# Optimization experiments

Hardware: AMD Instinct MI355X
Metric: run time of the kernel (lower is better)

Reference implementation:

```python
import jax, jax.numpy as jnp
import numpy as np

STRIDE = 4.0      # fpn_strides[0]
POOL = 7          # roi_align_size
SR = 2            # roi_align_sampling_ratio
NUM_CLASSES = 10
B, N = 2, 512
C, H, W = 256, 256, 256
OUT = 1024


def _bilinear(feat_hwc, y, x):
    # feat_hwc: [H, W, C]; y, x: [N, 7, 7, SR, SR] sample coords (feature units)
    Hf, Wf, _ = feat_hwc.shape
    valid = (y > -1.0) & (y < Hf) & (x > -1.0) & (x < Wf)
    y = jnp.clip(y, 0.0, Hf - 1.0)
    x = jnp.clip(x, 0.0, Wf - 1.0)
    y0 = jnp.floor(y)
    x0 = jnp.floor(x)
    y0i = y0.astype(jnp.int32)
    x0i = x0.astype(jnp.int32)
    y1i = jnp.minimum(y0i + 1, Hf - 1)
    x1i = jnp.minimum(x0i + 1, Wf - 1)
    ly = (y - y0)[..., None]
    lx = (x - x0)[..., None]
    hy = 1.0 - ly
    hx = 1.0 - lx
    v = (hy * hx * feat_hwc[y0i, x0i] + hy * lx * feat_hwc[y0i, x1i]
         + ly * hx * feat_hwc[y1i, x0i] + ly * lx * feat_hwc[y1i, x1i])
    return v * valid[..., None]


def _roi_align_rotated(feat_hwc, boxes):
    # boxes: [N, 5] = (cx, cy, w, h, theta) in feature coords -> [N, 7, 7, C]
    cx, cy, w, h, th = (boxes[:, k] for k in range(5))
    bins = jnp.arange(POOL, dtype=feat_hwc.dtype)
    sub = (jnp.arange(SR, dtype=feat_hwc.dtype) + 0.5) / SR
    # local (box-frame) coords of sample points along each axis: [N, 7, SR]
    ys = -h[:, None, None] / 2 + (h / POOL)[:, None, None] * (bins[None, :, None] + sub[None, None, :])
    xs = -w[:, None, None] / 2 + (w / POOL)[:, None, None] * (bins[None, :, None] + sub[None, None, :])
    yy = ys[:, :, None, :, None]  # [N,7,1,SR,1]
    xx = xs[:, None, :, None, :]  # [N,1,7,1,SR]
    cos = jnp.cos(th)[:, None, None, None, None]
    sin = jnp.sin(th)[:, None, None, None, None]
    gx = cx[:, None, None, None, None] + xx * cos - yy * sin
    gy = cy[:, None, None, None, None] + xx * sin + yy * cos
    v = _bilinear(feat_hwc, gy, gx)  # [N,7,7,SR,SR,C]
    return v.mean(axis=(3, 4))       # average-pool the SRxSR samples per bin


def norm_angle(a):
    return (a + jnp.pi / 2) % jnp.pi - jnp.pi / 2


def setup_inputs():
    key = jax.random.key(0)
    ks = jax.random.split(key, 14)
    feat = jax.random.normal(ks[0], (B, C, H, W), jnp.float32)
    cx = jax.random.uniform(ks[1], (B, N), minval=16.0, maxval=H - 16.0)
    cy = jax.random.uniform(ks[2], (B, N), minval=16.0, maxval=W - 16.0)
    bw = jax.random.uniform(ks[3], (B, N), minval=8.0, maxval=64.0)
    bh = jax.random.uniform(ks[4], (B, N), minval=8.0, maxval=64.0)
    th = jax.random.uniform(ks[5], (B, N), minval=-np.pi / 2, maxval=np.pi / 2)
    proposals = jnp.stack([cx, cy, bw, bh, th], axis=-1).astype(jnp.float32)
    d_in = C * POOL * POOL
    s = 0.02
    return {
        'feat': feat,
        'proposals': proposals,
        'W1': jax.random.normal(ks[6], (d_in, OUT), jnp.float32) * s,
        'b1': jnp.zeros((OUT,), jnp.float32),
        'W2': jax.random.normal(ks[7], (OUT, OUT), jnp.float32) * s,
        'b2': jnp.zeros((OUT,), jnp.float32),
        'Wcls': jax.random.normal(ks[8], (OUT, NUM_CLASSES + 1), jnp.float32) * s,
        'bcls': jnp.zeros((NUM_CLASSES + 1,), jnp.float32),
        'Wreg': jax.random.normal(ks[9], (OUT, 5), jnp.float32) * s,
        'breg': jnp.zeros((5,), jnp.float32),
    }


def reference(feat, proposals, W1, b1, W2, b2, Wcls, bcls, Wreg, breg):
    Bn, Nn = proposals.shape[:2]
    feat_hwc = jnp.transpose(feat, (0, 2, 3, 1))  # [B,H,W,C]
    pooled = jax.vmap(_roi_align_rotated)(feat_hwc, proposals)  # [B,N,7,7,C]
    # torch flattens [N, C, 7, 7] -> C*49; match that layout
    x = jnp.transpose(pooled, (0, 1, 4, 2, 3)).reshape(Bn, Nn, -1)
    x = jax.nn.relu(x @ W1 + b1)
    x = jax.nn.relu(x @ W2 + b2)
    cls = x @ Wcls + bcls   # [B,N,11]
    reg = x @ Wreg + breg   # [B,N,5]
    # decode (proposals scaled to image coords by stride; theta unscaled)
    scale = jnp.array([STRIDE, STRIDE, STRIDE, STRIDE, 1.0], feat.dtype)
    p = proposals * scale
    clamp_v = float(abs(np.log(16.0 / 1000.0)))
    bx = p[..., 2] * reg[..., 0] + p[..., 0]
    by = p[..., 3] * reg[..., 1] + p[..., 1]
    bw = p[..., 2] * jnp.exp(jnp.clip(reg[..., 2], -clamp_v, clamp_v))
    bh = p[..., 3] * jnp.exp(jnp.clip(reg[..., 3], -clamp_v, clamp_v))
    ba = norm_angle(p[..., 4] + reg[..., 4])
    boxes = jnp.stack([bx, by, bw, bh, ba], axis=-1)
    return boxes, cls
```

## Files before the change

kernel.cpp:

```cpp
#include <hip/hip_runtime.h>
#include <math.h>
#include <stdint.h>

#define BB 2
#define NN 512
#define CC 256
#define HH 256
#define WW 256
#define DIN 12544
#define OUT1 1024
#define NCLS 11
#define NROI 1024
#define SK1 8
#define SK2 2

typedef short bf16x8 __attribute__((ext_vector_type(8)));
typedef float f32x4 __attribute__((ext_vector_type(4)));

__device__ inline unsigned short f2bf(float f) {
  unsigned int u = __float_as_uint(f);
  u += 0x7FFF + ((u >> 16) & 1);
  return (unsigned short)(u >> 16);
}
__device__ inline float bf2f(unsigned short h) {
  return __uint_as_float(((unsigned int)h) << 16);
}
__device__ inline float4 ld_bf4(const unsigned short* p) {
  ushort4 r = *(const ushort4*)p;
  return make_float4(bf2f(r.x), bf2f(r.y), bf2f(r.z), bf2f(r.w));
}

__device__ inline void gll16(const void* g, void* l) {
  __builtin_amdgcn_global_load_lds(
      reinterpret_cast<const __attribute__((address_space(1))) void*>(
          reinterpret_cast<uintptr_t>(g)),
      reinterpret_cast<__attribute__((address_space(3))) void*>(
          (unsigned int)reinterpret_cast<uintptr_t>(l)),
      16, 0, 0);
}

__global__ __launch_bounds__(256) void transpose_to_hwc_bf16(
    const float* __restrict__ in, unsigned short* __restrict__ out) {
  __shared__ float tile[64][65];
  int b = blockIdx.z;
  int hw0 = blockIdx.x * 64;
  int c0 = blockIdx.y * 64;
  int tid = threadIdx.x;
  int hi = tid >> 4, lo = tid & 15;
#pragma unroll
  for (int pass = 0; pass < 4; ++pass) {
    int cl = hi + pass * 16;
    float4 v = *(const float4*)(in + ((size_t)b * CC + c0 + cl) * (HH * WW) +
                                hw0 + lo * 4);
    tile[lo * 4 + 0][cl] = v.x;
    tile[lo * 4 + 1][cl] = v.y;
    tile[lo * 4 + 2][cl] = v.z;
    tile[lo * 4 + 3][cl] = v.w;
  }
  __syncthreads();
#pragma unroll
  for (int pass = 0; pass < 4; ++pass) {
    int hwl = hi + pass * 16;
    int cc = lo * 4;
    ushort4 o;
    o.x = f2bf(tile[hwl][cc + 0]);
    o.y = f2bf(tile[hwl][cc + 1]);
    o.z = f2bf(tile[hwl][cc + 2]);
    o.w = f2bf(tile[hwl][cc + 3]);
    *(ushort4*)(out + ((size_t)b * (HH * WW) + hw0 + hwl) * CC + c0 + cc) = o;
  }
}

__device__ inline void bilin(float gy, float gx, int& y0, int& x0, int& y1,
                             int& x1, float& w00, float& w01, float& w10,
                             float& w11) {
  float valid = (gy > -1.f && gy < 256.f && gx > -1.f && gx < 256.f) ? 0.25f : 0.f;
  float y = fminf(fmaxf(gy, 0.f), 255.f);
  float x = fminf(fmaxf(gx, 0.f), 255.f);
  float yf = floorf(y), xf = floorf(x);
  y0 = (int)yf; x0 = (int)xf;
  y1 = min(y0 + 1, 255); x1 = min(x0 + 1, 255);
  float ly = y - yf, lx = x - xf, hy = 1.f - ly, hx = 1.f - lx;
  w00 = hy * hx * valid; w01 = hy * lx * valid;
  w10 = ly * hx * valid; w11 = ly * lx * valid;
}

__global__ __launch_bounds__(256) void roi_align_hwc(
    const unsigned short* __restrict__ fhwc, const float* __restrict__ props,
    unsigned short* __restrict__ pooled) {
  int roi = blockIdx.x;
  int b = roi >> 9;
  const float* p = props + (size_t)roi * 5;
  float cx = p[0], cy = p[1], w = p[2], h = p[3], th = p[4];
  float sn = sinf(th), cs = cosf(th);
  int wave = threadIdx.x >> 6, lane = threadIdx.x & 63;
  int c4 = lane * 4;
  const unsigned short* fb = fhwc + (size_t)b * HH * WW * CC;
  unsigned short* outp = pooled + (size_t)roi * DIN;

  for (int bin = wave; bin < 49; bin += 4) {
    int py = bin / 7, px = bin - py * 7;
    float a0 = 0.f, a1 = 0.f, a2 = 0.f, a3 = 0.f;
#pragma unroll
    for (int sy = 0; sy < 2; ++sy) {
#pragma unroll
      for (int sx = 0; sx < 2; ++sx) {
        float ys = -0.5f * h + (h / 7.0f) * ((float)py + ((float)sy + 0.5f) * 0.5f);
        float xs = -0.5f * w + (w / 7.0f) * ((float)px + ((float)sx + 0.5f) * 0.5f);
        float gx = cx + xs * cs - ys * sn;
        float gy = cy + xs * sn + ys * cs;
        int y0, x0, y1, x1; float w00, w01, w10, w11;
        bilin(gy, gx, y0, x0, y1, x1, w00, w01, w10, w11);
        float4 v00 = ld_bf4(fb + ((size_t)(y0 * WW + x0)) * CC + c4);
        float4 v01 = ld_bf4(fb + ((size_t)(y0 * WW + x1)) * CC + c4);
        float4 v10 = ld_bf4(fb + ((size_t)(y1 * WW + x0)) * CC + c4);
        float4 v11 = ld_bf4(fb + ((size_t)(y1 * WW + x1)) * CC + c4);
        a0 += w00 * v00.x + w01 * v01.x + w10 * v10.x + w11 * v11.x;
        a1 += w00 * v00.y + w01 * v01.y + w10 * v10.y + w11 * v11.y;
        a2 += w00 * v00.z + w01 * v01.z + w10 * v10.z + w11 * v11.z;
        a3 += w00 * v00.w + w01 * v01.w + w10 * v10.w + w11 * v11.w;
      }
    }
    ushort4 o;
    o.x = f2bf(a0); o.y = f2bf(a1); o.z = f2bf(a2); o.w = f2bf(a3);
    *(ushort4*)(outp + bin * 256 + c4) = o;
  }
}

__global__ __launch_bounds__(256) void roi_align_nchw(
    const float* __restrict__ feat, const float* __restrict__ props,
    unsigned short* __restrict__ pooled) {
  int roi = blockIdx.x;
  int b = roi >> 9;
  int c = threadIdx.x;
  const float* p = props + (size_t)roi * 5;
  float cx = p[0], cy = p[1], w = p[2], h = p[3], th = p[4];
  float sn = sinf(th), cs = cosf(th);
  const float* fb = feat + ((size_t)b * CC + c) * (HH * WW);
  unsigned short* outp = pooled + (size_t)roi * DIN;
  for (int bin = 0; bin < 49; ++bin) {
    int py = bin / 7, px = bin - py * 7;
    float acc = 0.f;
#pragma unroll
    for (int sy = 0; sy < 2; ++sy) {
#pragma unroll
      for (int sx = 0; sx < 2; ++sx) {
        float ys = -0.5f * h + (h / 7.0f) * ((float)py + ((float)sy + 0.5f) * 0.5f);
        float xs = -0.5f * w + (w / 7.0f) * ((float)px + ((float)sx + 0.5f) * 0.5f);
        float gx = cx + xs * cs - ys * sn;
        float gy = cy + xs * sn + ys * cs;
        int y0, x0, y1, x1; float w00, w01, w10, w11;
        bilin(gy, gx, y0, x0, y1, x1, w00, w01, w10, w11);
        acc += w00 * fb[(size_t)y0 * WW + x0] + w01 * fb[(size_t)y0 * WW + x1] +
               w10 * fb[(size_t)y1 * WW + x0] + w11 * fb[(size_t)y1 * WW + x1];
      }
    }
    outp[bin * 256 + c] = f2bf(acc);
  }
}

template <bool PERM>
__global__ __launch_bounds__(256) void cvt_w(const float* __restrict__ in,
                                             unsigned short* __restrict__ out,
                                             int N, int Kout) {
  __shared__ float tile[64][65];
  int k0 = blockIdx.x * 64, n0 = blockIdx.y * 64;
  int tid = threadIdx.x;
  int hi = tid >> 4, lo = tid & 15;
#pragma unroll
  for (int pass = 0; pass < 4; ++pass) {
    int ki = hi + pass * 16;
    int k = k0 + ki;
    int row = PERM ? ((k & 255) * 49 + (k >> 8)) : k;
    float4 v = *(const float4*)(in + (size_t)row * N + n0 + lo * 4);
    tile[ki][lo * 4 + 0] = v.x;
    tile[ki][lo * 4 + 1] = v.y;
    tile[ki][lo * 4 + 2] = v.z;
    tile[ki][lo * 4 + 3] = v.w;
  }
  __syncthreads();
#pragma unroll
  for (int pass = 0; pass < 4; ++pass) {
    int nl = hi + pass * 16;
    int kq = lo * 4;
    ushort4 o;
    o.x = f2bf(tile[kq + 0][nl]);
    o.y = f2bf(tile[kq + 1][nl]);
    o.z = f2bf(tile[kq + 2][nl]);
    o.w = f2bf(tile[kq + 3][nl]);
    *(ushort4*)(out + (size_t)(n0 + nl) * Kout + k0 + kq) = o;
  }
}

__global__ __launch_bounds__(256) void gemm_mfma_128(
    const unsigned short* __restrict__ A, const unsigned short* __restrict__ Bw,
    float* __restrict__ part, int K, int Ks) {
  __shared__ short As[128 * 32];
  __shared__ short Bs[128 * 32];
  int tid = threadIdx.x;
  int w = tid >> 6, lane = tid & 63;
  int quad = lane >> 4, l16 = lane & 15;
  int m0 = blockIdx.y * 128, n0 = blockIdx.x * 128;
  int bz = blockIdx.z;
  int wm = w >> 1, wn = w & 1;

  const char* pA = (const char*)A +
      ((size_t)(m0 + 32 * w + (lane >> 2)) * K + (size_t)bz * Ks) * 2 +
      (lane & 3) * 16;
  const char* pB = (const char*)Bw +
      ((size_t)(n0 + 32 * w + (lane >> 2)) * K + (size_t)bz * Ks) * 2 +
      (lane & 3) * 16;
  short* la = &As[w * 1024];
  short* lb = &Bs[w * 1024];
  const size_t rstep = (size_t)K * 2 * 16;

  f32x4 acc[4][4] = {};
  int aoff[4], boff[4];
#pragma unroll
  for (int t = 0; t < 4; ++t) {
    aoff[t] = (wm * 64 + t * 16 + l16) * 32 + quad * 8;
    boff[t] = (wn * 64 + t * 16 + l16) * 32 + quad * 8;
  }

  for (int kk = 0; kk < Ks; kk += 32) {
    __syncthreads();
    gll16(pA, la);
    gll16(pA + rstep, la + 512);
    gll16(pB, lb);
    gll16(pB + rstep, lb + 512);
    pA += 64; pB += 64;
    __syncthreads();
    bf16x8 af[4], bfr[4];
#pragma unroll
    for (int t = 0; t < 4; ++t) af[t] = *(const bf16x8*)&As[aoff[t]];
#pragma unroll
    for (int t = 0; t < 4; ++t) bfr[t] = *(const bf16x8*)&Bs[boff[t]];
#pragma unroll
    for (int mt = 0; mt < 4; ++mt)
#pragma unroll
      for (int nt = 0; nt < 4; ++nt)
        acc[mt][nt] = __builtin_amdgcn_mfma_f32_16x16x32_bf16(
            af[mt], bfr[nt], acc[mt][nt], 0, 0, 0);
  }

  float* pp = part + (size_t)bz * (OUT1 * NROI);
#pragma unroll
  for (int mt = 0; mt < 4; ++mt)
#pragma unroll
    for (int nt = 0; nt < 4; ++nt) {
      int col = n0 + wn * 64 + nt * 16 + l16;
#pragma unroll
      for (int r = 0; r < 4; ++r) {
        int row = m0 + wm * 64 + mt * 16 + quad * 4 + r;
        pp[(size_t)row * OUT1 + col] = acc[mt][nt][r];
      }
    }
}

__global__ __launch_bounds__(256) void reduce_relu_bf16(
    const float* __restrict__ part, const float* __restrict__ bias,
    unsigned short* __restrict__ out) {
  int i = blockIdx.x * 256 + threadIdx.x;
  int base = i * 4;
  int col = base & (OUT1 - 1);
  const float4* p = (const float4*)part;
  float4 s = p[i];
#pragma unroll
  for (int z = 1; z < SK1; ++z) {
    float4 t = p[i + (size_t)z * (NROI * OUT1 / 4)];
    s.x += t.x; s.y += t.y; s.z += t.z; s.w += t.w;
  }
  float4 bv = *(const float4*)(bias + col);
  ushort4 o;
  o.x = f2bf(fmaxf(s.x + bv.x, 0.f));
  o.y = f2bf(fmaxf(s.y + bv.y, 0.f));
  o.z = f2bf(fmaxf(s.z + bv.z, 0.f));
  o.w = f2bf(fmaxf(s.w + bv.w, 0.f));
  *(ushort4*)(out + base) = o;
}

__global__ __launch_bounds__(256) void gemm_mfma_64_part(
    const unsigned short* __restrict__ A, const unsigned short* __restrict__ Bw,
    float* __restrict__ part, int K, int Ks) {
  __shared__ short As[64 * 64];
  __shared__ short Bs[64 * 64];
  int tid = threadIdx.x;
  int w = tid >> 6, lane = tid & 63;
  int quad = lane >> 4, l16 = lane & 15;
  int m0 = blockIdx.y * 64, n0 = blockIdx.x * 64;
  int bz = blockIdx.z;
  int wm = w >> 1, wn = w & 1;

  const char* pA = (const char*)A +
      ((size_t)(m0 + 16 * w + (lane >> 3)) * K + (size_t)bz * Ks) * 2 +
      (lane & 7) * 16;
  const char* pB = (const char*)Bw +
      ((size_t)(n0 + 16 * w + (lane >> 3)) * K + (size_t)bz * Ks) * 2 +
      (lane & 7) * 16;
  short* la = &As[w * 1024];
  short* lb = &Bs[w * 1024];
  const size_t rstep = (size_t)K * 2 * 8;

  f32x4 acc[2][2] = {};
  int aoff[2], boff[2];
#pragma unroll
  for (int t = 0; t < 2; ++t) {
    aoff[t] = (wm * 32 + t * 16 + l16) * 64 + quad * 8;
    boff[t] = (wn * 32 + t * 16 + l16) * 64 + quad * 8;
  }

  for (int kk = 0; kk < Ks; kk += 64) {
    __syncthreads();
    gll16(pA, la);
    gll16(pA + rstep, la + 512);
    gll16(pB, lb);
    gll16(pB + rstep, lb + 512);
    pA += 128; pB += 128;
    __syncthreads();
#pragma unroll
    for (int ks = 0; ks < 2; ++ks) {
      bf16x8 af[2], bfr[2];
#pragma unroll
      for (int t = 0; t < 2; ++t) af[t] = *(const bf16x8*)&As[aoff[t] + ks * 32];
#pragma unroll
      for (int t = 0; t < 2; ++t) bfr[t] = *(const bf16x8*)&Bs[boff[t] + ks * 32];
#pragma unroll
      for (int mt = 0; mt < 2; ++mt)
#pragma unroll
        for (int nt = 0; nt < 2; ++nt)
          acc[mt][nt] = __builtin_amdgcn_mfma_f32_16x16x32_bf16(
              af[mt], bfr[nt], acc[mt][nt], 0, 0, 0);
    }
  }
  float* pp = part + (size_t)bz * (OUT1 * NROI);
#pragma unroll
  for (int mt = 0; mt < 2; ++mt)
#pragma unroll
    for (int nt = 0; nt < 2; ++nt) {
      int col = n0 + wn * 32 + nt * 16 + l16;
#pragma unroll
      for (int r = 0; r < 4; ++r) {
        int row = m0 + wm * 32 + mt * 16 + quad * 4 + r;
        pp[(size_t)row * OUT1 + col] = acc[mt][nt][r];
      }
    }
}

__global__ __launch_bounds__(256) void head_kernel(
    const float* __restrict__ P0, const float* __restrict__ P1,
    const float* __restrict__ b2, const float* __restrict__ Wcls,
    const float* __restrict__ bcls, const float* __restrict__ Wreg,
    const float* __restrict__ breg, const float* __restrict__ props,
    float* __restrict__ out) {
  __shared__ float xrow[1024];
  __shared__ float partial[16][17];
  __shared__ float res[16];
  int row = blockIdx.x;
  int tid = threadIdx.x;
  {
    size_t off = (size_t)row * 1024 + tid * 4;
    float4 a = *(const float4*)(P0 + off);
    float4 b = *(const float4*)(P1 + off);
    float4 bv = *(const float4*)(b2 + tid * 4);
    xrow[tid * 4 + 0] = fmaxf(a.x + b.x + bv.x, 0.f);
    xrow[tid * 4 + 1] = fmaxf(a.y + b.y + bv.y, 0.f);
    xrow[tid * 4 + 2] = fmaxf(a.z + b.z + bv.z, 0.f);
    xrow[tid * 4 + 3] = fmaxf(a.w + b.w + bv.w, 0.f);
  }
  __syncthreads();
  int col = tid & 15, slice = tid >> 4;
  float s = 0.f;
  if (col < NCLS) {
    for (int k = slice * 64; k < slice * 64 + 64; ++k)
      s += xrow[k] * Wcls[(size_t)k * NCLS + col];
  } else {
    int rc = col - NCLS;
    for (int k = slice * 64; k < slice * 64 + 64; ++k)
      s += xrow[k] * Wreg[(size_t)k * 5 + rc];
  }
  partial[slice][col] = s;
  __syncthreads();
  if (tid < 16) {
    float t = 0.f;
    for (int sl = 0; sl < 16; ++sl) t += partial[sl][tid];
    t += (tid < NCLS) ? bcls[tid] : breg[tid - NCLS];
    res[tid] = t;
  }
  __syncthreads();
  if (tid < NCLS) out[5120 + (size_t)row * NCLS + tid] = res[tid];
  if (tid == 0) {
    const float* p = props + (size_t)row * 5;
    float p0 = p[0] * 4.f, p1 = p[1] * 4.f, p2 = p[2] * 4.f, p3 = p[3] * 4.f,
          p4 = p[4];
    float r0 = res[11], r1 = res[12], r2 = res[13], r3 = res[14], r4 = res[15];
    const float V = 4.135166556742356f;
    float bx = p2 * r0 + p0;
    float by = p3 * r1 + p1;
    float bw = p2 * expf(fminf(fmaxf(r2, -V), V));
    float bh = p3 * expf(fminf(fmaxf(r3, -V), V));
    const float PI = 3.14159265358979323846f;
    float a = p4 + r4;
    float m = fmodf(a + PI * 0.5f, PI);
    if (m < 0.f) m += PI;
    float ba = m - PI * 0.5f;
    float* bo = out + (size_t)row * 5;
    bo[0] = bx; bo[1] = by; bo[2] = bw; bo[3] = bh; bo[4] = ba;
  }
}

extern "C" void kernel_launch(void* const* d_in, const int* in_sizes, int n_in,
                              void* d_out, int out_size, void* d_ws,
                              size_t ws_size, hipStream_t stream) {
  const float* feat  = (const float*)d_in[0];
  const float* props = (const float*)d_in[1];
  const float* W1    = (const float*)d_in[2];
  const float* b1    = (const float*)d_in[3];
  const float* W2    = (const float*)d_in[4];
  const float* b2    = (const float*)d_in[5];
  const float* Wcls  = (const float*)d_in[6];
  const float* bcls  = (const float*)d_in[7];
  const float* Wreg  = (const float*)d_in[8];
  const float* breg  = (const float*)d_in[9];
  float* out = (float*)d_out;

  char* wp = (char*)d_ws;
  unsigned short* pooled = (unsigned short*)wp; wp += (size_t)NROI * DIN * 2;
  unsigned short* W1T    = (unsigned short*)wp; wp += (size_t)OUT1 * DIN * 2;
  unsigned short* W2T    = (unsigned short*)wp; wp += (size_t)OUT1 * OUT1 * 2;
  unsigned short* x1     = (unsigned short*)wp; wp += (size_t)NROI * OUT1 * 2;
  float*          part1  = (float*)wp;          wp += (size_t)SK1 * NROI * OUT1 * 4;
  float*          part2  = (float*)wp;          wp += (size_t)SK2 * NROI * OUT1 * 4;
  unsigned short* fhwc   = (unsigned short*)wp;

  size_t need_min  = (size_t)(wp - (char*)d_ws);
  size_t need_full = need_min + (size_t)BB * CC * HH * WW * 2;

  if (ws_size >= need_full) {
    transpose_to_hwc_bf16<<<dim3(HH * WW / 64, CC / 64, BB), 256, 0, stream>>>(
        feat, fhwc);
    roi_align_hwc<<<NROI, 256, 0, stream>>>(fhwc, props, pooled);
  } else {
    roi_align_nchw<<<NROI, 256, 0, stream>>>(feat, props, pooled);
  }

  cvt_w<true><<<dim3(DIN / 64, OUT1 / 64), 256, 0, stream>>>(W1, W1T, OUT1, DIN);
  cvt_w<false><<<dim3(OUT1 / 64, OUT1 / 64), 256, 0, stream>>>(W2, W2T, OUT1, OUT1);

  gemm_mfma_128<<<dim3(8, 8, SK1), 256, 0, stream>>>(pooled, W1T, part1, DIN,
                                                     DIN / SK1);
  reduce_relu_bf16<<<NROI * OUT1 / 1024, 256, 0, stream>>>(part1, b1, x1);
  gemm_mfma_64_part<<<dim3(16, 16, SK2), 256, 0, stream>>>(x1, W2T, part2, OUT1,
                                                           OUT1 / SK2);
  head_kernel<<<NROI, 256, 0, stream>>>(part2, part2 + (size_t)NROI * OUT1, b2,
                                        Wcls, bcls, Wreg, breg, props, out);
}
```

Before: 388.7 us.

## Widen transpose/convert tiles, vectorize ROI gathers, and raise split-K factors

Several separate changes land together. The feature transpose and weight-convert kernels now use 128-wide tiles with 8 passes per block. ROI align gathers 8 bf16 channels per lane with 16-byte loads, so each wave covers two bins at once. The split-K factors for both GEMMs go up (8→14 and 2→4), and the head kernel now sums a variable number of partials. The aim is fewer, wider memory transactions and more GEMM parallelism, at the cost of larger fp32 partial buffers and more reduction traffic.

```diff
diff --git a/kernel.cpp b/kernel.cpp
--- a/kernel.cpp
+++ b/kernel.cpp
@@ -11,8 +11,8 @@
 #define OUT1 1024
 #define NCLS 11
 #define NROI 1024
-#define SK1 8
-#define SK2 2
+#define SK1 14
+#define SK2 4
 
 typedef short bf16x8 __attribute__((ext_vector_type(8)));
 typedef float f32x4 __attribute__((ext_vector_type(4)));
@@ -24,10 +24,6 @@
 }
 __device__ inline float bf2f(unsigned short h) {
   return __uint_as_float(((unsigned int)h) << 16);
-}
-__device__ inline float4 ld_bf4(const unsigned short* p) {
-  ushort4 r = *(const ushort4*)p;
-  return make_float4(bf2f(r.x), bf2f(r.y), bf2f(r.z), bf2f(r.w));
 }
 
 __device__ inline void gll16(const void* g, void* l) {
@@ -41,33 +37,34 @@
 
 __global__ __launch_bounds__(256) void transpose_to_hwc_bf16(
     const float* __restrict__ in, unsigned short* __restrict__ out) {
-  __shared__ float tile[64][65];
+  __shared__ float tile[64][133];
   int b = blockIdx.z;
-  int hw0 = blockIdx.x * 64;
+  int hw0 = blockIdx.x * 128;
   int c0 = blockIdx.y * 64;
   int tid = threadIdx.x;
-  int hi = tid >> 4, lo = tid & 15;
-#pragma unroll
-  for (int pass = 0; pass < 4; ++pass) {
-    int cl = hi + pass * 16;
-    float4 v = *(const float4*)(in + ((size_t)b * CC + c0 + cl) * (HH * WW) +
-                                hw0 + lo * 4);
-    tile[lo * 4 + 0][cl] = v.x;
-    tile[lo * 4 + 1][cl] = v.y;
-    tile[lo * 4 + 2][cl] = v.z;
-    tile[lo * 4 + 3][cl] = v.w;
+  int rl = tid & 31, rr = tid >> 5;
+#pragma unroll
+  for (int p = 0; p < 8; ++p) {
+    int c = rr + p * 8;
+    float4 v = *(const float4*)(in + ((size_t)b * CC + c0 + c) * (HH * WW) +
+                                hw0 + rl * 4);
+    tile[c][rl * 4 + 0] = v.x;
+    tile[c][rl * 4 + 1] = v.y;
+    tile[c][rl * 4 + 2] = v.z;
+    tile[c][rl * 4 + 3] = v.w;
   }
   __syncthreads();
-#pragma unroll
-  for (int pass = 0; pass < 4; ++pass) {
-    int hwl = hi + pass * 16;
-    int cc = lo * 4;
+  int wl = tid & 15, wr = tid >> 4;
+#pragma unroll
+  for (int p = 0; p < 8; ++p) {
+    int hwl = wr + p * 16;
+    int cq = wl * 4;
     ushort4 o;
-    o.x = f2bf(tile[hwl][cc + 0]);
-    o.y = f2bf(tile[hwl][cc + 1]);
-    o.z = f2bf(tile[hwl][cc + 2]);
-    o.w = f2bf(tile[hwl][cc + 3]);
-    *(ushort4*)(out + ((size_t)b * (HH * WW) + hw0 + hwl) * CC + c0 + cc) = o;
+    o.x = f2bf(tile[cq + 0][hwl]);
+    o.y = f2bf(tile[cq + 1][hwl]);
+    o.z = f2bf(tile[cq + 2][hwl]);
+    o.w = f2bf(tile[cq + 3][hwl]);
+    *(ushort4*)(out + ((size_t)b * (HH * WW) + hw0 + hwl) * CC + c0 + cq) = o;
   }
 }
 
@@ -85,6 +82,17 @@
   w10 = ly * hx * valid; w11 = ly * lx * valid;
 }
 
+__device__ inline void fma8(uint4 v, float w, float* acc) {
+  acc[0] += w * __uint_as_float(v.x << 16);
+  acc[1] += w * __uint_as_float(v.x & 0xFFFF0000u);
+  acc[2] += w * __uint_as_float(v.y << 16);
+  acc[3] += w * __uint_as_float(v.y & 0xFFFF0000u);
+  acc[4] += w * __uint_as_float(v.z << 16);
+  acc[5] += w * __uint_as_float(v.z & 0xFFFF0000u);
+  acc[6] += w * __uint_as_float(v.w << 16);
+  acc[7] += w * __uint_as_float(v.w & 0xFFFF0000u);
+}
+
 __global__ __launch_bounds__(256) void roi_align_hwc(
     const unsigned short* __restrict__ fhwc, const float* __restrict__ props,
     unsigned short* __restrict__ pooled) {
@@ -93,37 +101,45 @@
   const float* p = props + (size_t)roi * 5;
   float cx = p[0], cy = p[1], w = p[2], h = p[3], th = p[4];
   float sn = sinf(th), cs = cosf(th);
-  int wave = threadIdx.x >> 6, lane = threadIdx.x & 63;
-  int c4 = lane * 4;
+  int tid = threadIdx.x;
+  int wave = tid >> 6, lane = tid & 63;
+  int half = lane >> 5, c8 = (lane & 31) * 8;
   const unsigned short* fb = fhwc + (size_t)b * HH * WW * CC;
   unsigned short* outp = pooled + (size_t)roi * DIN;
 
-  for (int bin = wave; bin < 49; bin += 4) {
-    int py = bin / 7, px = bin - py * 7;
-    float a0 = 0.f, a1 = 0.f, a2 = 0.f, a3 = 0.f;
-#pragma unroll
-    for (int sy = 0; sy < 2; ++sy) {
-#pragma unroll
-      for (int sx = 0; sx < 2; ++sx) {
-        float ys = -0.5f * h + (h / 7.0f) * ((float)py + ((float)sy + 0.5f) * 0.5f);
-        float xs = -0.5f * w + (w / 7.0f) * ((float)px + ((float)sx + 0.5f) * 0.5f);
-        float gx = cx + xs * cs - ys * sn;
-        float gy = cy + xs * sn + ys * cs;
-        int y0, x0, y1, x1; float w00, w01, w10, w11;
-        bilin(gy, gx, y0, x0, y1, x1, w00, w01, w10, w11);
-        float4 v00 = ld_bf4(fb + ((size_t)(y0 * WW + x0)) * CC + c4);
-        float4 v01 = ld_bf4(fb + ((size_t)(y0 * WW + x1)) * CC + c4);
-        float4 v10 = ld_bf4(fb + ((size_t)(y1 * WW + x0)) * CC + c4);
-        float4 v11 = ld_bf4(fb + ((size_t)(y1 * WW + x1)) * CC + c4);
-        a0 += w00 * v00.x + w01 * v01.x + w10 * v10.x + w11 * v11.x;
-        a1 += w00 * v00.y + w01 * v01.y + w10 * v10.y + w11 * v11.y;
-        a2 += w00 * v00.z + w01 * v01.z + w10 * v10.z + w11 * v11.z;
-        a3 += w00 * v00.w + w01 * v01.w + w10 * v10.w + w11 * v11.w;
+  for (int bb = wave * 2; bb < 49; bb += 8) {
+    int bin = bb + half;
+    bool ok = bin < 49;
+    if (ok) {
+      int py = bin / 7, px = bin - py * 7;
+      float acc[8] = {};
+#pragma unroll
+      for (int sy = 0; sy < 2; ++sy) {
+#pragma unroll
+        for (int sx = 0; sx < 2; ++sx) {
+          float ys = -0.5f * h + (h / 7.0f) * ((float)py + ((float)sy + 0.5f) * 0.5f);
+          float xs = -0.5f * w + (w / 7.0f) * ((float)px + ((float)sx + 0.5f) * 0.5f);
+          float gx = cx + xs * cs - ys * sn;
+          float gy = cy + xs * sn + ys * cs;
+          int y0, x0, y1, x1; float w00, w01, w10, w11;
+          bilin(gy, gx, y0, x0, y1, x1, w00, w01, w10, w11);
+          uint4 v00 = *(const uint4*)(fb + ((size_t)(y0 * WW + x0)) * CC + c8);
+          uint4 v01 = *(const uint4*)(fb + ((size_t)(y0 * WW + x1)) * CC + c8);
+          uint4 v10 = *(const uint4*)(fb + ((size_t)(y1 * WW + x0)) * CC + c8);
+          uint4 v11 = *(const uint4*)(fb + ((size_t)(y1 * WW + x1)) * CC + c8);
+          fma8(v00, w00, acc);
+          fma8(v01, w01, acc);
+          fma8(v10, w10, acc);
+          fma8(v11, w11, acc);
+        }
       }
-    }
-    ushort4 o;
-    o.x = f2bf(a0); o.y = f2bf(a1); o.z = f2bf(a2); o.w = f2bf(a3);
-    *(ushort4*)(outp + bin * 256 + c4) = o;
+      uint4 o;
+      o.x = (unsigned int)f2bf(acc[0]) | ((unsigned int)f2bf(acc[1]) << 16);
+      o.y = (unsigned int)f2bf(acc[2]) | ((unsigned int)f2bf(acc[3]) << 16);
+      o.z = (unsigned int)f2bf(acc[4]) | ((unsigned int)f2bf(acc[5]) << 16);
+      o.w = (unsigned int)f2bf(acc[6]) | ((unsigned int)f2bf(acc[7]) << 16);
+      *(uint4*)(outp + bin * 256 + c8) = o;
+    }
   }
 }
 
@@ -163,26 +179,27 @@
 __global__ __launch_bounds__(256) void cvt_w(const float* __restrict__ in,
                                              unsigned short* __restrict__ out,
                                              int N, int Kout) {
-  __shared__ float tile[64][65];
-  int k0 = blockIdx.x * 64, n0 = blockIdx.y * 64;
-  int tid = threadIdx.x;
-  int hi = tid >> 4, lo = tid & 15;
-#pragma unroll
-  for (int pass = 0; pass < 4; ++pass) {
-    int ki = hi + pass * 16;
+  __shared__ float tile[64][133];
+  int k0 = blockIdx.x * 64, n0 = blockIdx.y * 128;
+  int tid = threadIdx.x;
+  int rl = tid & 31, rr = tid >> 5;
+#pragma unroll
+  for (int p = 0; p < 8; ++p) {
+    int ki = rr + p * 8;
     int k = k0 + ki;
     int row = PERM ? ((k & 255) * 49 + (k >> 8)) : k;
-    float4 v = *(const float4*)(in + (size_t)row * N + n0 + lo * 4);
-    tile[ki][lo * 4 + 0] = v.x;
-    tile[ki][lo * 4 + 1] = v.y;
-    tile[ki][lo * 4 + 2] = v.z;
-    tile[ki][lo * 4 + 3] = v.w;
+    float4 v = *(const float4*)(in + (size_t)row * N + n0 + rl * 4);
+    tile[ki][rl * 4 + 0] = v.x;
+    tile[ki][rl * 4 + 1] = v.y;
+    tile[ki][rl * 4 + 2] = v.z;
+    tile[ki][rl * 4 + 3] = v.w;
   }
   __syncthreads();
-#pragma unroll
-  for (int pass = 0; pass < 4; ++pass) {
-    int nl = hi + pass * 16;
-    int kq = lo * 4;
+  int wl = tid & 15, wr = tid >> 4;
+#pragma unroll
+  for (int p = 0; p < 8; ++p) {
+    int nl = wr + p * 16;
+    int kq = wl * 4;
     ushort4 o;
     o.x = f2bf(tile[kq + 0][nl]);
     o.y = f2bf(tile[kq + 1][nl]);
@@ -347,11 +364,10 @@
 }
 
 __global__ __launch_bounds__(256) void head_kernel(
-    const float* __restrict__ P0, const float* __restrict__ P1,
-    const float* __restrict__ b2, const float* __restrict__ Wcls,
-    const float* __restrict__ bcls, const float* __restrict__ Wreg,
-    const float* __restrict__ breg, const float* __restrict__ props,
-    float* __restrict__ out) {
+    const float* __restrict__ P, const float* __restrict__ b2,
+    const float* __restrict__ Wcls, const float* __restrict__ bcls,
+    const float* __restrict__ Wreg, const float* __restrict__ breg,
+    const float* __restrict__ props, float* __restrict__ out) {
   __shared__ float xrow[1024];
   __shared__ float partial[16][17];
   __shared__ float res[16];
@@ -359,13 +375,17 @@
   int tid = threadIdx.x;
   {
     size_t off = (size_t)row * 1024 + tid * 4;
-    float4 a = *(const float4*)(P0 + off);
-    float4 b = *(const float4*)(P1 + off);
+    float4 a = *(const float4*)(P + off);
+#pragma unroll
+    for (int z = 1; z < SK2; ++z) {
+      float4 t = *(const float4*)(P + (size_t)z * (NROI * OUT1) + off);
+      a.x += t.x; a.y += t.y; a.z += t.z; a.w += t.w;
+    }
     float4 bv = *(const float4*)(b2 + tid * 4);
-    xrow[tid * 4 + 0] = fmaxf(a.x + b.x + bv.x, 0.f);
-    xrow[tid * 4 + 1] = fmaxf(a.y + b.y + bv.y, 0.f);
-    xrow[tid * 4 + 2] = fmaxf(a.z + b.z + bv.z, 0.f);
-    xrow[tid * 4 + 3] = fmaxf(a.w + b.w + bv.w, 0.f);
+    xrow[tid * 4 + 0] = fmaxf(a.x + bv.x, 0.f);
+    xrow[tid * 4 + 1] = fmaxf(a.y + bv.y, 0.f);
+    xrow[tid * 4 + 2] = fmaxf(a.z + bv.z, 0.f);
+    xrow[tid * 4 + 3] = fmaxf(a.w + bv.w, 0.f);
   }
   __syncthreads();
   int col = tid & 15, slice = tid >> 4;
@@ -436,21 +456,22 @@
   size_t need_full = need_min + (size_t)BB * CC * HH * WW * 2;
 
   if (ws_size >= need_full) {
-    transpose_to_hwc_bf16<<<dim3(HH * WW / 64, CC / 64, BB), 256, 0, stream>>>(
+    transpose_to_hwc_bf16<<<dim3(HH * WW / 128, CC / 64, BB), 256, 0, stream>>>(
         feat, fhwc);
     roi_align_hwc<<<NROI, 256, 0, stream>>>(fhwc, props, pooled);
   } else {
     roi_align_nchw<<<NROI, 256, 0, stream>>>(feat, props, pooled);
   }
 
-  cvt_w<true><<<dim3(DIN / 64, OUT1 / 64), 256, 0, stream>>>(W1, W1T, OUT1, DIN);
-  cvt_w<false><<<dim3(OUT1 / 64, OUT1 / 64), 256, 0, stream>>>(W2, W2T, OUT1, OUT1);
+  cvt_w<true><<<dim3(DIN / 64, OUT1 / 128), 256, 0, stream>>>(W1, W1T, OUT1, DIN);
+  cvt_w<false><<<dim3(OUT1 / 64, OUT1 / 128), 256, 0, stream>>>(W2, W2T, OUT1,
+                                                                OUT1);
 
   gemm_mfma_128<<<dim3(8, 8, SK1), 256, 0, stream>>>(pooled, W1T, part1, DIN,
                                                      DIN / SK1);
   reduce_relu_bf16<<<NROI * OUT1 / 1024, 256, 0, stream>>>(part1, b1, x1);
   gemm_mfma_64_part<<<dim3(16, 16, SK2), 256, 0, stream>>>(x1, W2T, part2, OUT1,
                                                            OUT1 / SK2);
-  head_kernel<<<NROI, 256, 0, stream>>>(part2, part2 + (size_t)NROI * OUT1, b2,
-                                        Wcls, bcls, Wreg, breg, props, out);
-}
+  head_kernel<<<NROI, 256, 0, stream>>>(part2, b2, Wcls, bcls, Wreg, breg,
+                                        props, out);
+}
```

After: 395.5 us. About the same (+1.8%).
